# Kernel optimization log

Measured on AMD Instinct MI355X. Metric: run time of the kernel, lower is better.

The kernel has to match this reference:

```python
import jax, jax.numpy as jnp
import numpy as np

N = 16384   # nodes
E = 262144  # edges (avg degree 16)
H = 256     # hidden_dim
R = 32      # num_radial


def _lin(k, fi, fo):
    return jax.random.normal(k, (fi, fo), jnp.float32) / np.float32(np.sqrt(fi))


def setup_inputs() -> dict:
    key = jax.random.key(0)
    ks = jax.random.split(key, 16)
    h = jax.random.normal(ks[0], (N, H), jnp.float32)
    pos = jax.random.normal(ks[1], (N, 3), jnp.float32)
    edge_index = jax.random.randint(ks[2], (2, E), 0, N, dtype=jnp.int32)
    return {
        'h': h, 'pos': pos,
        # radial_basis: Linear(1,R), SiLU, Linear(R,R)
        'rb_w1': _lin(ks[3], 1, R), 'rb_b1': jnp.zeros((R,), jnp.float32),
        'rb_w2': _lin(ks[4], R, R), 'rb_b2': jnp.zeros((R,), jnp.float32),
        # edge_network: Linear(2H+R,H), SiLU, Linear(H,H), LayerNorm(H)
        'en_w1': _lin(ks[5], 2 * H + R, H), 'en_b1': jnp.zeros((H,), jnp.float32),
        'en_w2': _lin(ks[6], H, H), 'en_b2': jnp.zeros((H,), jnp.float32),
        'en_g': jnp.ones((H,), jnp.float32), 'en_bt': jnp.zeros((H,), jnp.float32),
        # node_network: Linear(2H,H), SiLU, Linear(H,H), LayerNorm(H)
        'nn_w1': _lin(ks[7], 2 * H, H), 'nn_b1': jnp.zeros((H,), jnp.float32),
        'nn_w2': _lin(ks[8], H, H), 'nn_b2': jnp.zeros((H,), jnp.float32),
        'nn_g': jnp.ones((H,), jnp.float32), 'nn_bt': jnp.zeros((H,), jnp.float32),
        # coord_network: Linear(H,H//2), SiLU, Linear(H//2,1), Tanh
        'cn_w1': _lin(ks[9], H, H // 2), 'cn_b1': jnp.zeros((H // 2,), jnp.float32),
        'cn_w2': _lin(ks[10], H // 2, 1), 'cn_b2': jnp.zeros((1,), jnp.float32),
        'edge_index': edge_index,
    }


def _ln(x, g, b, eps=1e-5):
    mu = jnp.mean(x, axis=-1, keepdims=True)
    var = jnp.var(x, axis=-1, keepdims=True)
    return (x - mu) / jnp.sqrt(var + eps) * g + b


def reference(h, pos, rb_w1, rb_b1, rb_w2, rb_b2,
              en_w1, en_b1, en_w2, en_b2, en_g, en_bt,
              nn_w1, nn_b1, nn_w2, nn_b2, nn_g, nn_bt,
              cn_w1, cn_b1, cn_w2, cn_b2, edge_index):
    row, col = edge_index[0], edge_index[1]
    rel_pos = pos[col] - pos[row]                                   # [E,3]
    # torch: norm(rel_pos + 1e-8) -> scalar eps added to the vector first
    dist = jnp.linalg.norm(rel_pos + 1e-8, axis=-1, keepdims=True)  # [E,1]
    radial = jax.nn.silu(dist @ rb_w1 + rb_b1) @ rb_w2 + rb_b2      # [E,R]
    edge_feat = jnp.concatenate([h[row], h[col], radial], axis=-1)  # [E,2H+R]
    edge_msg = _ln(jax.nn.silu(edge_feat @ en_w1 + en_b1) @ en_w2 + en_b2,
                   en_g, en_bt)                                     # [E,H]
    # PyG propagate with aggr='add': sum messages at target nodes (col)
    node_msg = jax.ops.segment_sum(edge_msg, col, num_segments=h.shape[0])
    hn_in = jnp.concatenate([h, node_msg], axis=-1)                 # [N,2H]
    h_updated = _ln(jax.nn.silu(hn_in @ nn_w1 + nn_b1) @ nn_w2 + nn_b2,
                    nn_g, nn_bt)                                    # [N,H]
    coord_w = jnp.tanh(jax.nn.silu(edge_msg @ cn_w1 + cn_b1) @ cn_w2 + cn_b2)  # [E,1]
    weighted = rel_pos * coord_w                                    # [E,3]
    pos_updates = jnp.zeros_like(pos).at[row].add(-weighted).at[col].add(weighted)
    return h_updated, pos_updates
```

## Files before the change

kernel.cpp:

```cpp
#include <hip/hip_runtime.h>
#include <hip/hip_bf16.h>


#define NN 16384
#define EE 262144
#define HH 256
#define RR 32

typedef __bf16 bf16x8 __attribute__((ext_vector_type(8)));
typedef float f32x4 __attribute__((ext_vector_type(4)));

__device__ __forceinline__ float silu_f(float x) { return x / (1.0f + __expf(-x)); }

__device__ __forceinline__ unsigned short bf_bits(float x) {
  union { __hip_bfloat16 b; unsigned short u; } v;
  v.b = __float2bfloat16(x);
  return v.u;
}
__device__ __forceinline__ float ubf(unsigned short u) {
  return __uint_as_float(((unsigned)u) << 16);
}

__global__ __launch_bounds__(256) void conv_h_kernel(const float* __restrict__ src,
                                                     __hip_bfloat16* __restrict__ dst,
                                                     int n4) {
  int i = blockIdx.x * 256 + threadIdx.x;
  if (i >= n4) return;
  float4 v = ((const float4*)src)[i];
  __hip_bfloat16* d = dst + (size_t)i * 4;
  d[0] = __float2bfloat16(v.x);
  d[1] = __float2bfloat16(v.y);
  d[2] = __float2bfloat16(v.z);
  d[3] = __float2bfloat16(v.w);
}

__global__ __launch_bounds__(256) void tr_kernel(const float* __restrict__ in,
                                                 __hip_bfloat16* __restrict__ out,
                                                 int K, int Nc) {
  int i = blockIdx.x * 256 + threadIdx.x;
  if (i >= K * Nc) return;
  int k = i / Nc, c = i - k * Nc;
  out[(size_t)c * K + k] = __float2bfloat16(in[i]);
}

__global__ __launch_bounds__(256) void rwt_kernel(const float* __restrict__ rb_w2,
                                                  const float* __restrict__ en_w1,
                                                  __hip_bfloat16* __restrict__ RWT) {
  int t = blockIdx.x * 256 + threadIdx.x;
  if (t >= 256 * 32) return;
  int c = t >> 5, i = t & 31;
  float s = 0.f;
#pragma unroll
  for (int j = 0; j < 32; ++j) s += rb_w2[i * 32 + j] * en_w1[(512 + j) * 256 + c];
  RWT[c * 32 + i] = __float2bfloat16(s);
}

__global__ __launch_bounds__(256) void b1p_kernel(const float* __restrict__ en_b1,
                                                  const float* __restrict__ rb_b2,
                                                  const float* __restrict__ en_w1,
                                                  float* __restrict__ b1p) {
  int c = blockIdx.x * 256 + threadIdx.x;
  if (c >= 256) return;
  float s = en_b1[c];
#pragma unroll
  for (int j = 0; j < 32; ++j) s += rb_b2[j] * en_w1[(512 + j) * 256 + c];
  b1p[c] = s;
}

__global__ __launch_bounds__(256) void count_kernel(const int* __restrict__ ei,
                                                    int* __restrict__ counts) {
  int e = blockIdx.x * 256 + threadIdx.x;
  if (e >= EE) return;
  atomicAdd(&counts[ei[EE + e]], 1);
}

__global__ __launch_bounds__(256) void scanA_kernel(const int* __restrict__ counts,
                                                    int* __restrict__ bsum) {
  __shared__ int ws[4];
  int t = threadIdx.x;
  int v = counts[blockIdx.x * 256 + t];
#pragma unroll
  for (int m = 1; m < 64; m <<= 1) v += __shfl_xor(v, m, 64);
  if ((t & 63) == 0) ws[t >> 6] = v;
  __syncthreads();
  if (t == 0) bsum[blockIdx.x] = ws[0] + ws[1] + ws[2] + ws[3];
}

__global__ __launch_bounds__(64) void scanB_kernel(const int* __restrict__ bsum,
                                                   int* __restrict__ bbase,
                                                   int* __restrict__ offs) {
  int t = threadIdx.x;
  int v = bsum[t], x = v;
#pragma unroll
  for (int d = 1; d < 64; d <<= 1) {
    int y = __shfl_up(x, d, 64);
    if (t >= d) x += y;
  }
  bbase[t] = x - v;
  if (t == 63) offs[NN] = x;
}

__global__ __launch_bounds__(256) void scanC_kernel(const int* __restrict__ counts,
                                                    const int* __restrict__ bbase,
                                                    int* __restrict__ offs,
                                                    int* __restrict__ cursor) {
  __shared__ int wtot[4];
  int t = threadIdx.x, wv = t >> 6, ln = t & 63;
  int base = blockIdx.x * 256;
  int v = counts[base + t], x = v;
#pragma unroll
  for (int d = 1; d < 64; d <<= 1) {
    int y = __shfl_up(x, d, 64);
    if (ln >= d) x += y;
  }
  if (ln == 63) wtot[wv] = x;
  __syncthreads();
  int add = bbase[blockIdx.x];
  for (int k = 0; k < wv; ++k) add += wtot[k];
  int excl = add + x - v;
  offs[base + t] = excl;
  cursor[base + t] = excl;
}

__global__ __launch_bounds__(256) void scatter_kernel(const int* __restrict__ ei,
                                                      int* __restrict__ cursor,
                                                      int* __restrict__ elist) {
  int e = blockIdx.x * 256 + threadIdx.x;
  if (e >= EE) return;
  int c = ei[EE + e];
  int p = atomicAdd(&cursor[c], 1);
  elist[p] = e;
}

__global__ __launch_bounds__(512) void pgemm_kernel(const __hip_bfloat16* __restrict__ A,
                                                    const __hip_bfloat16* __restrict__ BT,
                                                    __hip_bfloat16* __restrict__ out) {
  const int tid = threadIdx.x, w = tid >> 6, l = tid & 63, r = l & 15, g = l >> 4;
  const int n0 = blockIdx.x * 64;
  f32x4 acc[4][4];
#pragma unroll
  for (int a = 0; a < 4; ++a)
#pragma unroll
    for (int b = 0; b < 4; ++b) acc[a][b] = (f32x4){0.f, 0.f, 0.f, 0.f};
  for (int ks = 0; ks < 8; ++ks) {
    bf16x8 af[4], bfr[4];
#pragma unroll
    for (int fm = 0; fm < 4; ++fm)
      af[fm] = *(const bf16x8*)(A + (size_t)(n0 + fm * 16 + r) * 256 + ks * 32 + g * 8);
#pragma unroll
    for (int fn = 0; fn < 4; ++fn)
      bfr[fn] = *(const bf16x8*)(BT + (size_t)(w * 64 + fn * 16 + r) * 256 + ks * 32 + g * 8);
#pragma unroll
    for (int fm = 0; fm < 4; ++fm)
#pragma unroll
      for (int fn = 0; fn < 4; ++fn)
        acc[fm][fn] =
            __builtin_amdgcn_mfma_f32_16x16x32_bf16(af[fm], bfr[fn], acc[fm][fn], 0, 0, 0);
  }
#pragma unroll
  for (int fm = 0; fm < 4; ++fm)
#pragma unroll
    for (int fn = 0; fn < 4; ++fn) {
      int col = w * 64 + fn * 16 + r;
#pragma unroll
      for (int q = 0; q < 4; ++q) {
        int row = n0 + fm * 16 + g * 4 + q;
        out[(size_t)row * 512 + col] = __float2bfloat16(acc[fm][fn][q]);
      }
    }
}

__global__ __launch_bounds__(512, 4) void edge_kernel(
    const __hip_bfloat16* __restrict__ Pb, const int* __restrict__ ei,
    const float* __restrict__ pos, const float* __restrict__ rb_w1,
    const float* __restrict__ rb_b1, const __hip_bfloat16* __restrict__ RWT,
    const float* __restrict__ b1p, const __hip_bfloat16* __restrict__ W2T,
    const float* __restrict__ en_b2, const float* __restrict__ en_g,
    const float* __restrict__ en_bt, const __hip_bfloat16* __restrict__ CW1T,
    const float* __restrict__ cn_b1, const float* __restrict__ cn_w2,
    const float* __restrict__ cn_b2, const int* __restrict__ elist,
    __hip_bfloat16* __restrict__ emsg, float* __restrict__ pos_out) {
  __shared__ __align__(16) __hip_bfloat16 A2[64 * 264];
  __shared__ float relb[64][3];
  __shared__ float distb[64];
  __shared__ int srow[64], scol[64];
  __shared__ float red[8][64], redsq[8][64];
  __shared__ float mv[64][2];
  __shared__ float cb1b[128], cw2b[128];

  const int tid = threadIdx.x, w = tid >> 6, l = tid & 63, r = l & 15, g = l >> 4;
  const int e0 = blockIdx.x * 64;

  if (tid < 128) {
    cb1b[tid] = cn_b1[tid];
    cw2b[tid] = cn_w2[tid];
  }
  if (tid < 64) {
    int e = elist[e0 + tid];
    int r2 = ei[e], c2 = ei[EE + e];
    srow[tid] = r2;
    scol[tid] = c2;
    float dx = pos[c2 * 3 + 0] - pos[r2 * 3 + 0];
    float dy = pos[c2 * 3 + 1] - pos[r2 * 3 + 1];
    float dz = pos[c2 * 3 + 2] - pos[r2 * 3 + 2];
    relb[tid][0] = dx;
    relb[tid][1] = dy;
    relb[tid][2] = dz;
    float ex = dx + 1e-8f, ey = dy + 1e-8f, ez = dz + 1e-8f;
    distb[tid] = sqrtf(ex * ex + ey * ey + ez * ez);
  }
  __syncthreads();

  unsigned short* A2u = (unsigned short*)A2;
  {
    const int eloc = (w & 3) * 16 + r;
    const int chalf = w >> 2;
    float d = distb[eloc];
    bf16x8 sfrag;
#pragma unroll
    for (int j = 0; j < 8; ++j) {
      float x = d * rb_w1[g * 8 + j] + rb_b1[g * 8 + j];
      sfrag[j] = (__bf16)silu_f(x);
    }
#pragma unroll
    for (int t = 0; t < 8; ++t) {
      int cblk = chalf * 8 + t;
      int cbase = cblk * 16 + g * 4;
      bf16x8 afr = *(const bf16x8*)(RWT + (size_t)(cblk * 16 + r) * 32 + g * 8);
      f32x4 rad = __builtin_amdgcn_mfma_f32_16x16x32_bf16(
          afr, sfrag, (f32x4){0.f, 0.f, 0.f, 0.f}, 0, 0, 0);
      ushort4 o;
      o.x = bf_bits(rad[0]);
      o.y = bf_bits(rad[1]);
      o.z = bf_bits(rad[2]);
      o.w = bf_bits(rad[3]);
      *(ushort4*)(A2u + (size_t)eloc * 264 + cbase) = o;
    }
  }
  __syncthreads();

#pragma unroll
  for (int it = 0; it < 4; ++it) {
    int ch = it * 512 + tid;
    int i = ch >> 5, c = ch & 31;
    bf16x8 radv = *(const bf16x8*)(A2 + i * 264 + c * 8);
    bf16x8 p1 = *(const bf16x8*)(Pb + (size_t)srow[i] * 512 + c * 8);
    bf16x8 p2 = *(const bf16x8*)(Pb + (size_t)scol[i] * 512 + 256 + c * 8);
    float4 b1a = *(const float4*)(b1p + c * 8);
    float4 b1b = *(const float4*)(b1p + c * 8 + 4);
    float bv[8] = {b1a.x, b1a.y, b1a.z, b1a.w, b1b.x, b1b.y, b1b.z, b1b.w};
    bf16x8 o;
#pragma unroll
    for (int j = 0; j < 8; ++j)
      o[j] = (__bf16)silu_f((float)radv[j] + (float)p1[j] + (float)p2[j] + bv[j]);
    *(bf16x8*)(A2 + i * 264 + c * 8) = o;
  }
  __syncthreads();

  f32x4 acc[2][4];
#pragma unroll
  for (int a = 0; a < 2; ++a)
#pragma unroll
    for (int b = 0; b < 4; ++b) acc[a][b] = (f32x4){0.f, 0.f, 0.f, 0.f};
  for (int ks = 0; ks < 8; ++ks) {
    bf16x8 af[2], bfr[4];
#pragma unroll
    for (int mf = 0; mf < 2; ++mf)
      af[mf] = *(const bf16x8*)(W2T + (size_t)(w * 32 + mf * 16 + r) * 256 + ks * 32 + g * 8);
#pragma unroll
    for (int nf = 0; nf < 4; ++nf)
      bfr[nf] = *(const bf16x8*)(A2 + (nf * 16 + r) * 264 + ks * 32 + g * 8);
#pragma unroll
    for (int mf = 0; mf < 2; ++mf)
#pragma unroll
      for (int nf = 0; nf < 4; ++nf)
        acc[mf][nf] =
            __builtin_amdgcn_mfma_f32_16x16x32_bf16(af[mf], bfr[nf], acc[mf][nf], 0, 0, 0);
  }
  {
    float4 b2v0 = *(const float4*)(en_b2 + w * 32 + g * 4);
    float4 b2v1 = *(const float4*)(en_b2 + w * 32 + 16 + g * 4);
#pragma unroll
    for (int nf = 0; nf < 4; ++nf) {
      acc[0][nf][0] += b2v0.x;
      acc[0][nf][1] += b2v0.y;
      acc[0][nf][2] += b2v0.z;
      acc[0][nf][3] += b2v0.w;
      acc[1][nf][0] += b2v1.x;
      acc[1][nf][1] += b2v1.y;
      acc[1][nf][2] += b2v1.z;
      acc[1][nf][3] += b2v1.w;
    }
  }

#pragma unroll
  for (int nf = 0; nf < 4; ++nf) {
    float s = 0.f, sq = 0.f;
#pragma unroll
    for (int mf = 0; mf < 2; ++mf)
#pragma unroll
      for (int q = 0; q < 4; ++q) {
        float v = acc[mf][nf][q];
        s += v;
        sq += v * v;
      }
    s += __shfl_xor(s, 16, 64);
    s += __shfl_xor(s, 32, 64);
    sq += __shfl_xor(sq, 16, 64);
    sq += __shfl_xor(sq, 32, 64);
    if (l < 16) {
      red[w][nf * 16 + l] = s;
      redsq[w][nf * 16 + l] = sq;
    }
  }
  __syncthreads();
  if (tid < 64) {
    float s = 0.f, sq = 0.f;
#pragma unroll
    for (int k = 0; k < 8; ++k) {
      s += red[k][tid];
      sq += redsq[k][tid];
    }
    float mean = s * (1.0f / HH);
    float var = sq * (1.0f / HH) - mean * mean;
    mv[tid][0] = mean;
    mv[tid][1] = rsqrtf(var + 1e-5f);
  }
  __syncthreads();

  {
    float4 gv0 = *(const float4*)(en_g + w * 32 + g * 4);
    float4 gv1 = *(const float4*)(en_g + w * 32 + 16 + g * 4);
    float4 bv0 = *(const float4*)(en_bt + w * 32 + g * 4);
    float4 bv1 = *(const float4*)(en_bt + w * 32 + 16 + g * 4);
#pragma unroll
    for (int nf = 0; nf < 4; ++nf) {
      int e = nf * 16 + r;
      float mm = mv[e][0], rs = mv[e][1];
      ushort4 o0, o1;
      o0.x = bf_bits((acc[0][nf][0] - mm) * rs * gv0.x + bv0.x);
      o0.y = bf_bits((acc[0][nf][1] - mm) * rs * gv0.y + bv0.y);
      o0.z = bf_bits((acc[0][nf][2] - mm) * rs * gv0.z + bv0.z);
      o0.w = bf_bits((acc[0][nf][3] - mm) * rs * gv0.w + bv0.w);
      o1.x = bf_bits((acc[1][nf][0] - mm) * rs * gv1.x + bv1.x);
      o1.y = bf_bits((acc[1][nf][1] - mm) * rs * gv1.y + bv1.y);
      o1.z = bf_bits((acc[1][nf][2] - mm) * rs * gv1.z + bv1.z);
      o1.w = bf_bits((acc[1][nf][3] - mm) * rs * gv1.w + bv1.w);
      *(ushort4*)(A2u + (size_t)e * 264 + w * 32 + g * 4) = o0;
      *(ushort4*)(A2u + (size_t)e * 264 + w * 32 + 16 + g * 4) = o1;
    }
  }
  __syncthreads();

#pragma unroll
  for (int it = 0; it < 4; ++it) {
    int ch = it * 512 + tid;
    int i = ch >> 5, c = ch & 31;
    *(float4*)(emsg + (size_t)(e0 + i) * HH + c * 8) = *(const float4*)(A2 + i * 264 + c * 8);
  }

  f32x4 c2a[4];
#pragma unroll
  for (int a = 0; a < 4; ++a) c2a[a] = (f32x4){0.f, 0.f, 0.f, 0.f};
  for (int ks = 0; ks < 8; ++ks) {
    bf16x8 af[4];
#pragma unroll
    for (int fm = 0; fm < 4; ++fm)
      af[fm] = *(const bf16x8*)(A2 + (fm * 16 + r) * 264 + ks * 32 + g * 8);
    bf16x8 bfr = *(const bf16x8*)(CW1T + (size_t)(w * 16 + r) * 256 + ks * 32 + g * 8);
#pragma unroll
    for (int fm = 0; fm < 4; ++fm)
      c2a[fm] = __builtin_amdgcn_mfma_f32_16x16x32_bf16(af[fm], bfr, c2a[fm], 0, 0, 0);
  }
  {
    int ccol = w * 16 + r;
    float cb = cb1b[ccol], cw = cw2b[ccol];
#pragma unroll
    for (int fm = 0; fm < 4; ++fm)
#pragma unroll
      for (int q = 0; q < 4; ++q) {
        float v = silu_f(c2a[fm][q] + cb) * cw;
#pragma unroll
        for (int m = 1; m < 16; m <<= 1) v += __shfl_xor(v, m, 64);
        if (r == 0) red[w][fm * 16 + g * 4 + q] = v;
      }
  }
  __syncthreads();
  if (tid < 64) {
    float s = cn_b2[0];
#pragma unroll
    for (int k = 0; k < 8; ++k) s += red[k][tid];
    float wgt = tanhf(s);
    float ax = relb[tid][0], ay = relb[tid][1], az = relb[tid][2];
    int rr = srow[tid], cc = scol[tid];
    atomicAdd(&pos_out[rr * 3 + 0], -wgt * ax);
    atomicAdd(&pos_out[rr * 3 + 1], -wgt * ay);
    atomicAdd(&pos_out[rr * 3 + 2], -wgt * az);
    atomicAdd(&pos_out[cc * 3 + 0], wgt * ax);
    atomicAdd(&pos_out[cc * 3 + 1], wgt * ay);
    atomicAdd(&pos_out[cc * 3 + 2], wgt * az);
  }
}

__global__ __launch_bounds__(256) void nodemsg_kernel(const int* __restrict__ offs,
                                                      const __hip_bfloat16* __restrict__ emsg,
                                                      __hip_bfloat16* __restrict__ nmsgb) {
  int wid = threadIdx.x >> 6, l = threadIdx.x & 63;
  int n = blockIdx.x * 4 + wid;
  float a0 = 0.f, a1 = 0.f, a2 = 0.f, a3 = 0.f;
  int b = offs[n], e2 = offs[n + 1];
  const unsigned short* E = (const unsigned short*)emsg;
  int p = b;
  for (; p + 1 < e2; p += 2) {
    ushort4 va = *(const ushort4*)(E + (size_t)p * HH + l * 4);
    ushort4 vb = *(const ushort4*)(E + (size_t)(p + 1) * HH + l * 4);
    a0 += ubf(va.x) + ubf(vb.x);
    a1 += ubf(va.y) + ubf(vb.y);
    a2 += ubf(va.z) + ubf(vb.z);
    a3 += ubf(va.w) + ubf(vb.w);
  }
  if (p < e2) {
    ushort4 va = *(const ushort4*)(E + (size_t)p * HH + l * 4);
    a0 += ubf(va.x);
    a1 += ubf(va.y);
    a2 += ubf(va.z);
    a3 += ubf(va.w);
  }
  ushort4 o;
  o.x = bf_bits(a0);
  o.y = bf_bits(a1);
  o.z = bf_bits(a2);
  o.w = bf_bits(a3);
  *(ushort4*)((unsigned short*)nmsgb + (size_t)n * HH + l * 4) = o;
}

__global__ __launch_bounds__(512, 4) void node_kernel(
    const __hip_bfloat16* __restrict__ hb, const __hip_bfloat16* __restrict__ nmsgb,
    const __hip_bfloat16* __restrict__ NW1T, const float* __restrict__ nn_b1,
    const __hip_bfloat16* __restrict__ NW2T, const float* __restrict__ nn_b2,
    const float* __restrict__ nn_g, const float* __restrict__ nn_bt,
    float* __restrict__ out_h) {
  __shared__ __align__(16) __hip_bfloat16 A2[32 * 264];
  __shared__ float red[8][32], redsq[8][32];
  __shared__ float mv[32][2];
  __shared__ float gb[HH], btb[HH];
  const int tid = threadIdx.x, w = tid >> 6, l = tid & 63, r = l & 15, g = l >> 4;
  const int n0 = blockIdx.x * 32;
  if (tid < 256) {
    gb[tid] = nn_g[tid];
    btb[tid] = nn_bt[tid];
  }

  f32x4 acc[2][2];
#pragma unroll
  for (int a = 0; a < 2; ++a)
#pragma unroll
    for (int b = 0; b < 2; ++b) acc[a][b] = (f32x4){0.f, 0.f, 0.f, 0.f};
  for (int ks = 0; ks < 8; ++ks) {
    bf16x8 af[2], bfr[2];
#pragma unroll
    for (int fm = 0; fm < 2; ++fm)
      af[fm] = *(const bf16x8*)(hb + (size_t)(n0 + fm * 16 + r) * 256 + ks * 32 + g * 8);
#pragma unroll
    for (int fn = 0; fn < 2; ++fn)
      bfr[fn] = *(const bf16x8*)(NW1T + (size_t)(w * 32 + fn * 16 + r) * 512 + ks * 32 + g * 8);
#pragma unroll
    for (int fm = 0; fm < 2; ++fm)
#pragma unroll
      for (int fn = 0; fn < 2; ++fn)
        acc[fm][fn] =
            __builtin_amdgcn_mfma_f32_16x16x32_bf16(af[fm], bfr[fn], acc[fm][fn], 0, 0, 0);
  }
  for (int ks = 0; ks < 8; ++ks) {
    bf16x8 af[2], bfr[2];
#pragma unroll
    for (int fm = 0; fm < 2; ++fm)
      af[fm] = *(const bf16x8*)(nmsgb + (size_t)(n0 + fm * 16 + r) * 256 + ks * 32 + g * 8);
#pragma unroll
    for (int fn = 0; fn < 2; ++fn)
      bfr[fn] =
          *(const bf16x8*)(NW1T + (size_t)(w * 32 + fn * 16 + r) * 512 + 256 + ks * 32 + g * 8);
#pragma unroll
    for (int fm = 0; fm < 2; ++fm)
#pragma unroll
      for (int fn = 0; fn < 2; ++fn)
        acc[fm][fn] =
            __builtin_amdgcn_mfma_f32_16x16x32_bf16(af[fm], bfr[fn], acc[fm][fn], 0, 0, 0);
  }
  __syncthreads();
#pragma unroll
  for (int fn = 0; fn < 2; ++fn) {
    int col = w * 32 + fn * 16 + r;
    float b1 = nn_b1[col];
#pragma unroll
    for (int fm = 0; fm < 2; ++fm)
#pragma unroll
      for (int q = 0; q < 4; ++q) {
        int row = fm * 16 + g * 4 + q;
        A2[row * 264 + col] = __float2bfloat16(silu_f(acc[fm][fn][q] + b1));
      }
  }
  __syncthreads();

#pragma unroll
  for (int a = 0; a < 2; ++a)
#pragma unroll
    for (int b = 0; b < 2; ++b) acc[a][b] = (f32x4){0.f, 0.f, 0.f, 0.f};
  for (int ks = 0; ks < 8; ++ks) {
    bf16x8 af[2], bfr[2];
#pragma unroll
    for (int fm = 0; fm < 2; ++fm)
      af[fm] = *(const bf16x8*)(A2 + (fm * 16 + r) * 264 + ks * 32 + g * 8);
#pragma unroll
    for (int fn = 0; fn < 2; ++fn)
      bfr[fn] = *(const bf16x8*)(NW2T + (size_t)(w * 32 + fn * 16 + r) * 256 + ks * 32 + g * 8);
#pragma unroll
    for (int fm = 0; fm < 2; ++fm)
#pragma unroll
      for (int fn = 0; fn < 2; ++fn)
        acc[fm][fn] =
            __builtin_amdgcn_mfma_f32_16x16x32_bf16(af[fm], bfr[fn], acc[fm][fn], 0, 0, 0);
  }
#pragma unroll
  for (int fn = 0; fn < 2; ++fn) {
    float b2 = nn_b2[w * 32 + fn * 16 + r];
#pragma unroll
    for (int fm = 0; fm < 2; ++fm)
#pragma unroll
      for (int q = 0; q < 4; ++q) acc[fm][fn][q] += b2;
  }
#pragma unroll
  for (int fm = 0; fm < 2; ++fm)
#pragma unroll
    for (int q = 0; q < 4; ++q) {
      float s = acc[fm][0][q] + acc[fm][1][q];
      float sq = acc[fm][0][q] * acc[fm][0][q] + acc[fm][1][q] * acc[fm][1][q];
#pragma unroll
      for (int m = 1; m < 16; m <<= 1) {
        s += __shfl_xor(s, m, 64);
        sq += __shfl_xor(sq, m, 64);
      }
      if (r == 0) {
        red[w][fm * 16 + g * 4 + q] = s;
        redsq[w][fm * 16 + g * 4 + q] = sq;
      }
    }
  __syncthreads();
  if (tid < 32) {
    float s = 0.f, sq = 0.f;
#pragma unroll
    for (int k = 0; k < 8; ++k) {
      s += red[k][tid];
      sq += redsq[k][tid];
    }
    float mean = s * (1.0f / HH);
    float var = sq * (1.0f / HH) - mean * mean;
    mv[tid][0] = mean;
    mv[tid][1] = rsqrtf(var + 1e-5f);
  }
  __syncthreads();
#pragma unroll
  for (int fn = 0; fn < 2; ++fn) {
    int col = w * 32 + fn * 16 + r;
    float gg = gb[col], bb = btb[col];
#pragma unroll
    for (int fm = 0; fm < 2; ++fm)
#pragma unroll
      for (int q = 0; q < 4; ++q) {
        int row = fm * 16 + g * 4 + q;
        out_h[(size_t)(n0 + row) * HH + col] =
            (acc[fm][fn][q] - mv[row][0]) * mv[row][1] * gg + bb;
      }
  }
}

extern "C" void kernel_launch(void* const* d_in, const int* in_sizes, int n_in,
                              void* d_out, int out_size, void* d_ws, size_t ws_size,
                              hipStream_t stream) {
  const float* h = (const float*)d_in[0];
  const float* pos = (const float*)d_in[1];
  const float* rb_w1 = (const float*)d_in[2];
  const float* rb_b1 = (const float*)d_in[3];
  const float* rb_w2 = (const float*)d_in[4];
  const float* rb_b2 = (const float*)d_in[5];
  const float* en_w1 = (const float*)d_in[6];
  const float* en_b1 = (const float*)d_in[7];
  const float* en_w2 = (const float*)d_in[8];
  const float* en_b2 = (const float*)d_in[9];
  const float* en_g = (const float*)d_in[10];
  const float* en_bt = (const float*)d_in[11];
  const float* nn_w1 = (const float*)d_in[12];
  const float* nn_b1 = (const float*)d_in[13];
  const float* nn_w2 = (const float*)d_in[14];
  const float* nn_b2 = (const float*)d_in[15];
  const float* nn_g = (const float*)d_in[16];
  const float* nn_bt = (const float*)d_in[17];
  const float* cn_w1 = (const float*)d_in[18];
  const float* cn_b1 = (const float*)d_in[19];
  const float* cn_w2 = (const float*)d_in[20];
  const float* cn_b2 = (const float*)d_in[21];
  const int* ei = (const int*)d_in[22];

  float* out_h = (float*)d_out;
  float* out_pos = out_h + (size_t)NN * HH;

  char* p = (char*)d_ws;
  auto alloc = [&p](size_t bytes) {
    char* q = p;
    p += (bytes + 255) & ~(size_t)255;
    return q;
  };
  __hip_bfloat16* hb = (__hip_bfloat16*)alloc((size_t)NN * HH * 2);
  __hip_bfloat16* Pb = (__hip_bfloat16*)alloc((size_t)NN * 512 * 2);
  __hip_bfloat16* W1abT = (__hip_bfloat16*)alloc((size_t)512 * 256 * 2);
  __hip_bfloat16* W2T = (__hip_bfloat16*)alloc((size_t)256 * 256 * 2);
  __hip_bfloat16* NW1T = (__hip_bfloat16*)alloc((size_t)256 * 512 * 2);
  __hip_bfloat16* NW2T = (__hip_bfloat16*)alloc((size_t)256 * 256 * 2);
  __hip_bfloat16* CW1T = (__hip_bfloat16*)alloc((size_t)128 * 256 * 2);
  __hip_bfloat16* RWT = (__hip_bfloat16*)alloc((size_t)256 * 32 * 2);
  float* b1p = (float*)alloc((size_t)256 * 4);
  __hip_bfloat16* emsg = (__hip_bfloat16*)alloc((size_t)EE * HH * 2);
  __hip_bfloat16* nmsgb = (__hip_bfloat16*)alloc((size_t)NN * HH * 2);
  int* counts = (int*)alloc((size_t)NN * 4);
  int* offs = (int*)alloc((size_t)(NN + 1) * 4);
  int* cursor = (int*)alloc((size_t)NN * 4);
  int* elist = (int*)alloc((size_t)EE * 4);
  int* bsum = (int*)alloc((size_t)64 * 4);
  int* bbase = (int*)alloc((size_t)64 * 4);

  hipMemsetAsync(out_pos, 0, (size_t)NN * 3 * sizeof(float), stream);
  hipMemsetAsync(counts, 0, (size_t)NN * sizeof(int), stream);

  conv_h_kernel<<<(NN * HH / 4 + 255) / 256, 256, 0, stream>>>(h, hb, NN * HH / 4);
  tr_kernel<<<(256 * 256) / 256, 256, 0, stream>>>(en_w2, W2T, 256, 256);
  tr_kernel<<<(512 * 256) / 256, 256, 0, stream>>>(nn_w1, NW1T, 512, 256);
  tr_kernel<<<(256 * 256) / 256, 256, 0, stream>>>(nn_w2, NW2T, 256, 256);
  tr_kernel<<<(256 * 128) / 256, 256, 0, stream>>>(cn_w1, CW1T, 256, 128);
  tr_kernel<<<(256 * 256) / 256, 256, 0, stream>>>(en_w1, W1abT, 256, 256);
  tr_kernel<<<(256 * 256) / 256, 256, 0, stream>>>(en_w1 + 256 * 256, W1abT + 256 * 256, 256,
                                                   256);
  rwt_kernel<<<(256 * 32) / 256, 256, 0, stream>>>(rb_w2, en_w1, RWT);
  b1p_kernel<<<1, 256, 0, stream>>>(en_b1, rb_b2, en_w1, b1p);
  count_kernel<<<EE / 256, 256, 0, stream>>>(ei, counts);
  scanA_kernel<<<NN / 256, 256, 0, stream>>>(counts, bsum);
  scanB_kernel<<<1, 64, 0, stream>>>(bsum, bbase, offs);
  scanC_kernel<<<NN / 256, 256, 0, stream>>>(counts, bbase, offs, cursor);
  scatter_kernel<<<EE / 256, 256, 0, stream>>>(ei, cursor, elist);
  pgemm_kernel<<<NN / 64, 512, 0, stream>>>(hb, W1abT, Pb);
  edge_kernel<<<EE / 64, 512, 0, stream>>>(Pb, ei, pos, rb_w1, rb_b1, RWT, b1p, W2T, en_b2,
                                           en_g, en_bt, CW1T, cn_b1, cn_w2, cn_b2, elist,
                                           emsg, out_pos);
  nodemsg_kernel<<<NN / 4, 256, 0, stream>>>(offs, emsg, nmsgb);
  node_kernel<<<NN / 32, 512, 0, stream>>>(hb, nmsgb, NW1T, nn_b1, NW2T, nn_b2, nn_g, nn_bt,
                                           out_h);
}
```

Measured before the change: 513.0 us.

## Fuse segment-sum into edge kernel and merge weight prep launches

The edge kernel now reduces its 64 edge messages by destination node directly into an fp32 node-message buffer. Since edges are sorted by destination, runs of equal nodes are summed in registers, interior runs are stored plainly and boundary runs are added atomically. This removes the bf16 edge-message buffer (E×H) write and reread, along with the separate nodemsg kernel. Eight weight-prep launches are also merged into one kernel. In exchange it adds a memset of the fp32 node buffer, float atomics, fp32 reads in the node kernel, and a serial 32-row scan per thread.

```diff
diff --git a/kernel.cpp b/kernel.cpp
--- a/kernel.cpp
+++ b/kernel.cpp
@@ -34,37 +34,48 @@
   d[3] = __float2bfloat16(v.w);
 }
 
-__global__ __launch_bounds__(256) void tr_kernel(const float* __restrict__ in,
-                                                 __hip_bfloat16* __restrict__ out,
-                                                 int K, int Nc) {
-  int i = blockIdx.x * 256 + threadIdx.x;
-  if (i >= K * Nc) return;
-  int k = i / Nc, c = i - k * Nc;
-  out[(size_t)c * K + k] = __float2bfloat16(in[i]);
-}
-
-__global__ __launch_bounds__(256) void rwt_kernel(const float* __restrict__ rb_w2,
-                                                  const float* __restrict__ en_w1,
-                                                  __hip_bfloat16* __restrict__ RWT) {
-  int t = blockIdx.x * 256 + threadIdx.x;
-  if (t >= 256 * 32) return;
-  int c = t >> 5, i = t & 31;
-  float s = 0.f;
-#pragma unroll
-  for (int j = 0; j < 32; ++j) s += rb_w2[i * 32 + j] * en_w1[(512 + j) * 256 + c];
-  RWT[c * 32 + i] = __float2bfloat16(s);
-}
-
-__global__ __launch_bounds__(256) void b1p_kernel(const float* __restrict__ en_b1,
-                                                  const float* __restrict__ rb_b2,
-                                                  const float* __restrict__ en_w1,
-                                                  float* __restrict__ b1p) {
-  int c = blockIdx.x * 256 + threadIdx.x;
-  if (c >= 256) return;
-  float s = en_b1[c];
-#pragma unroll
-  for (int j = 0; j < 32; ++j) s += rb_b2[j] * en_w1[(512 + j) * 256 + c];
-  b1p[c] = s;
+__global__ __launch_bounds__(256) void prep_w_kernel(
+    const float* __restrict__ en_w1, const float* __restrict__ en_w2,
+    const float* __restrict__ nn_w1, const float* __restrict__ nn_w2,
+    const float* __restrict__ cn_w1, const float* __restrict__ rb_w2,
+    const float* __restrict__ rb_b2, const float* __restrict__ en_b1,
+    __hip_bfloat16* __restrict__ W2T, __hip_bfloat16* __restrict__ NW1T,
+    __hip_bfloat16* __restrict__ NW2T, __hip_bfloat16* __restrict__ CW1T,
+    __hip_bfloat16* __restrict__ W1abT, __hip_bfloat16* __restrict__ RWT,
+    float* __restrict__ b1p) {
+  int bid = blockIdx.x, tid = threadIdx.x;
+  if (bid < 256) {
+    int i = bid * 256 + tid, k = i >> 8, c = i & 255;
+    W2T[(size_t)c * 256 + k] = __float2bfloat16(en_w2[i]);
+  } else if (bid < 768) {
+    int i = (bid - 256) * 256 + tid, k = i >> 8, c = i & 255;
+    NW1T[(size_t)c * 512 + k] = __float2bfloat16(nn_w1[i]);
+  } else if (bid < 1024) {
+    int i = (bid - 768) * 256 + tid, k = i >> 8, c = i & 255;
+    NW2T[(size_t)c * 256 + k] = __float2bfloat16(nn_w2[i]);
+  } else if (bid < 1152) {
+    int i = (bid - 1024) * 256 + tid, k = i >> 7, c = i & 127;
+    CW1T[(size_t)c * 256 + k] = __float2bfloat16(cn_w1[i]);
+  } else if (bid < 1408) {
+    int i = (bid - 1152) * 256 + tid, k = i >> 8, c = i & 255;
+    W1abT[(size_t)c * 256 + k] = __float2bfloat16(en_w1[i]);
+  } else if (bid < 1664) {
+    int i = (bid - 1408) * 256 + tid, k = i >> 8, c = i & 255;
+    W1abT[(size_t)(256 + c) * 256 + k] = __float2bfloat16(en_w1[256 * 256 + i]);
+  } else if (bid < 1696) {
+    int t = (bid - 1664) * 256 + tid;
+    int c = t >> 5, i = t & 31;
+    float s = 0.f;
+#pragma unroll
+    for (int j = 0; j < 32; ++j) s += rb_w2[i * 32 + j] * en_w1[(512 + j) * 256 + c];
+    RWT[c * 32 + i] = __float2bfloat16(s);
+  } else {
+    int c = tid;
+    float s = en_b1[c];
+#pragma unroll
+    for (int j = 0; j < 32; ++j) s += rb_b2[j] * en_w1[(512 + j) * 256 + c];
+    b1p[c] = s;
+  }
 }
 
 __global__ __launch_bounds__(256) void count_kernel(const int* __restrict__ ei,
@@ -179,7 +190,7 @@
     const float* __restrict__ en_bt, const __hip_bfloat16* __restrict__ CW1T,
     const float* __restrict__ cn_b1, const float* __restrict__ cn_w2,
     const float* __restrict__ cn_b2, const int* __restrict__ elist,
-    __hip_bfloat16* __restrict__ emsg, float* __restrict__ pos_out) {
+    float* __restrict__ nmsg, float* __restrict__ pos_out) {
   __shared__ __align__(16) __hip_bfloat16 A2[64 * 264];
   __shared__ float relb[64][3];
   __shared__ float distb[64];
@@ -352,11 +363,27 @@
   }
   __syncthreads();
 
-#pragma unroll
-  for (int it = 0; it < 4; ++it) {
-    int ch = it * 512 + tid;
-    int i = ch >> 5, c = ch & 31;
-    *(float4*)(emsg + (size_t)(e0 + i) * HH + c * 8) = *(const float4*)(A2 + i * 264 + c * 8);
+  {
+    int c = tid & 255, h = tid >> 8;
+    int rbeg = h * 32, rend = rbeg + 32;
+    int segstart = rbeg;
+    int cur = scol[rbeg];
+    float run = 0.f;
+    for (int row = rbeg; row < rend; ++row) {
+      int nd = scol[row];
+      if (nd != cur) {
+        float* dst = &nmsg[(size_t)cur * 256 + c];
+        if (segstart > rbeg)
+          *dst = run;
+        else
+          atomicAdd(dst, run);
+        segstart = row;
+        cur = nd;
+        run = 0.f;
+      }
+      run += ubf(A2u[(size_t)row * 264 + c]);
+    }
+    atomicAdd(&nmsg[(size_t)cur * 256 + c], run);
   }
 
   f32x4 c2a[4];
@@ -402,40 +429,8 @@
   }
 }
 
-__global__ __launch_bounds__(256) void nodemsg_kernel(const int* __restrict__ offs,
-                                                      const __hip_bfloat16* __restrict__ emsg,
-                                                      __hip_bfloat16* __restrict__ nmsgb) {
-  int wid = threadIdx.x >> 6, l = threadIdx.x & 63;
-  int n = blockIdx.x * 4 + wid;
-  float a0 = 0.f, a1 = 0.f, a2 = 0.f, a3 = 0.f;
-  int b = offs[n], e2 = offs[n + 1];
-  const unsigned short* E = (const unsigned short*)emsg;
-  int p = b;
-  for (; p + 1 < e2; p += 2) {
-    ushort4 va = *(const ushort4*)(E + (size_t)p * HH + l * 4);
-    ushort4 vb = *(const ushort4*)(E + (size_t)(p + 1) * HH + l * 4);
-    a0 += ubf(va.x) + ubf(vb.x);
-    a1 += ubf(va.y) + ubf(vb.y);
-    a2 += ubf(va.z) + ubf(vb.z);
-    a3 += ubf(va.w) + ubf(vb.w);
-  }
-  if (p < e2) {
-    ushort4 va = *(const ushort4*)(E + (size_t)p * HH + l * 4);
-    a0 += ubf(va.x);
-    a1 += ubf(va.y);
-    a2 += ubf(va.z);
-    a3 += ubf(va.w);
-  }
-  ushort4 o;
-  o.x = bf_bits(a0);
-  o.y = bf_bits(a1);
-  o.z = bf_bits(a2);
-  o.w = bf_bits(a3);
-  *(ushort4*)((unsigned short*)nmsgb + (size_t)n * HH + l * 4) = o;
-}
-
 __global__ __launch_bounds__(512, 4) void node_kernel(
-    const __hip_bfloat16* __restrict__ hb, const __hip_bfloat16* __restrict__ nmsgb,
+    const __hip_bfloat16* __restrict__ hb, const float* __restrict__ nmsg,
     const __hip_bfloat16* __restrict__ NW1T, const float* __restrict__ nn_b1,
     const __hip_bfloat16* __restrict__ NW2T, const float* __restrict__ nn_b2,
     const float* __restrict__ nn_g, const float* __restrict__ nn_bt,
@@ -474,8 +469,21 @@
   for (int ks = 0; ks < 8; ++ks) {
     bf16x8 af[2], bfr[2];
 #pragma unroll
-    for (int fm = 0; fm < 2; ++fm)
-      af[fm] = *(const bf16x8*)(nmsgb + (size_t)(n0 + fm * 16 + r) * 256 + ks * 32 + g * 8);
+    for (int fm = 0; fm < 2; ++fm) {
+      const float* src = nmsg + (size_t)(n0 + fm * 16 + r) * 256 + ks * 32 + g * 8;
+      float4 a0 = *(const float4*)src;
+      float4 a1 = *(const float4*)(src + 4);
+      bf16x8 v;
+      v[0] = (__bf16)a0.x;
+      v[1] = (__bf16)a0.y;
+      v[2] = (__bf16)a0.z;
+      v[3] = (__bf16)a0.w;
+      v[4] = (__bf16)a1.x;
+      v[5] = (__bf16)a1.y;
+      v[6] = (__bf16)a1.z;
+      v[7] = (__bf16)a1.w;
+      af[fm] = v;
+    }
 #pragma unroll
     for (int fn = 0; fn < 2; ++fn)
       bfr[fn] =
@@ -619,8 +627,7 @@
   __hip_bfloat16* CW1T = (__hip_bfloat16*)alloc((size_t)128 * 256 * 2);
   __hip_bfloat16* RWT = (__hip_bfloat16*)alloc((size_t)256 * 32 * 2);
   float* b1p = (float*)alloc((size_t)256 * 4);
-  __hip_bfloat16* emsg = (__hip_bfloat16*)alloc((size_t)EE * HH * 2);
-  __hip_bfloat16* nmsgb = (__hip_bfloat16*)alloc((size_t)NN * HH * 2);
+  float* nmsg = (float*)alloc((size_t)NN * HH * 4);
   int* counts = (int*)alloc((size_t)NN * 4);
   int* offs = (int*)alloc((size_t)(NN + 1) * 4);
   int* cursor = (int*)alloc((size_t)NN * 4);
@@ -630,17 +637,11 @@
 
   hipMemsetAsync(out_pos, 0, (size_t)NN * 3 * sizeof(float), stream);
   hipMemsetAsync(counts, 0, (size_t)NN * sizeof(int), stream);
-
+  hipMemsetAsync(nmsg, 0, (size_t)NN * HH * sizeof(float), stream);
+
+  prep_w_kernel<<<1697, 256, 0, stream>>>(en_w1, en_w2, nn_w1, nn_w2, cn_w1, rb_w2, rb_b2,
+                                          en_b1, W2T, NW1T, NW2T, CW1T, W1abT, RWT, b1p);
   conv_h_kernel<<<(NN * HH / 4 + 255) / 256, 256, 0, stream>>>(h, hb, NN * HH / 4);
-  tr_kernel<<<(256 * 256) / 256, 256, 0, stream>>>(en_w2, W2T, 256, 256);
-  tr_kernel<<<(512 * 256) / 256, 256, 0, stream>>>(nn_w1, NW1T, 512, 256);
-  tr_kernel<<<(256 * 256) / 256, 256, 0, stream>>>(nn_w2, NW2T, 256, 256);
-  tr_kernel<<<(256 * 128) / 256, 256, 0, stream>>>(cn_w1, CW1T, 256, 128);
-  tr_kernel<<<(256 * 256) / 256, 256, 0, stream>>>(en_w1, W1abT, 256, 256);
-  tr_kernel<<<(256 * 256) / 256, 256, 0, stream>>>(en_w1 + 256 * 256, W1abT + 256 * 256, 256,
-                                                   256);
-  rwt_kernel<<<(256 * 32) / 256, 256, 0, stream>>>(rb_w2, en_w1, RWT);
-  b1p_kernel<<<1, 256, 0, stream>>>(en_b1, rb_b2, en_w1, b1p);
   count_kernel<<<EE / 256, 256, 0, stream>>>(ei, counts);
   scanA_kernel<<<NN / 256, 256, 0, stream>>>(counts, bsum);
   scanB_kernel<<<1, 64, 0, stream>>>(bsum, bbase, offs);
@@ -649,8 +650,7 @@
   pgemm_kernel<<<NN / 64, 512, 0, stream>>>(hb, W1abT, Pb);
   edge_kernel<<<EE / 64, 512, 0, stream>>>(Pb, ei, pos, rb_w1, rb_b1, RWT, b1p, W2T, en_b2,
                                            en_g, en_bt, CW1T, cn_b1, cn_w2, cn_b2, elist,
-                                           emsg, out_pos);
-  nodemsg_kernel<<<NN / 4, 256, 0, stream>>>(offs, emsg, nmsgb);
-  node_kernel<<<NN / 32, 512, 0, stream>>>(hb, nmsgb, NW1T, nn_b1, NW2T, nn_b2, nn_g, nn_bt,
+                                           nmsg, out_pos);
+  node_kernel<<<NN / 32, 512, 0, stream>>>(hb, nmsg, NW1T, nn_b1, NW2T, nn_b2, nn_g, nn_bt,
                                            out_h);
 }
```

After: 492.1 us. 4.1% less time.
